# Performance work log

Hardware: AMD Instinct MI355X
Metric: run time of the kernel (lower is better)

## Reference

```python
import jax, jax.numpy as jnp
import numpy as np

BSZ, ILEN, TLEN = 64, 256, 64
IDIM, HDIM, ODIM = 512, 1024, 128


def setup_inputs() -> dict:
    key = jax.random.key(0)
    k1, k2, k3, k4 = jax.random.split(key, 4)
    # xavier-uniform-like scales (exact init values don't matter for correctness)
    def xavier(k, shape):
        fan_in, fan_out = shape[1], shape[0]
        lim = (6.0 / (fan_in + fan_out)) ** 0.5
        return jax.random.uniform(k, shape, jnp.float32, -lim, lim)
    return {
        "inp": jax.random.normal(k1, (BSZ, ILEN, IDIM), jnp.float32),
        "tlen": TLEN,
        "w_ih": xavier(k2, (4 * HDIM, IDIM)),
        "w_hh": xavier(k3, (4 * HDIM, HDIM)),
        "b": jnp.zeros((4 * HDIM,), jnp.float32),
        "clf_w": xavier(k4, (ODIM, HDIM)),
        "clf_b": jnp.zeros((ODIM,), jnp.float32),
    }


def _lstm_forward(inp, tlen, w_ih, w_hh, b, clf_w, clf_b):
    bsz, ilen, _ = inp.shape
    hdim = w_hh.shape[1]
    # pad tlen zero timesteps at the end (matches F.pad [0,0,0,tlen])
    inp_padded = jnp.pad(inp, ((0, 0), (0, tlen), (0, 0)))
    # precompute input projection for all timesteps: [B, T, 4H]
    x_proj = jnp.einsum("bti,gi->btg", inp_padded, w_ih) + b
    x_proj_t = jnp.swapaxes(x_proj, 0, 1)  # [T, B, 4H]

    def step(carry, xg):
        h, c = carry
        gates = xg + h @ w_hh.T  # [B, 4H]
        i, f, g, o = jnp.split(gates, 4, axis=-1)
        i = jax.nn.sigmoid(i)
        f = jax.nn.sigmoid(f)
        g = jnp.tanh(g)
        o = jax.nn.sigmoid(o)
        c_new = f * c + i * g
        h_new = o * jnp.tanh(c_new)
        return (h_new, c_new), h_new

    h0 = jnp.zeros((bsz, hdim), inp.dtype)
    c0 = jnp.zeros((bsz, hdim), inp.dtype)
    _, hs = jax.lax.scan(step, (h0, c0), x_proj_t)  # hs: [T, B, H]
    hs = jnp.swapaxes(hs, 0, 1)  # [B, T, H]
    probs = jax.nn.sigmoid(jnp.einsum("bth,oh->bto", hs, clf_w) + clf_b)
    return probs[:, ilen:]


def reference(inp, tlen, w_ih, w_hh, b, clf_w, clf_b):
    return _lstm_forward(inp, tlen, w_ih, w_hh, b, clf_w, clf_b)
```

## Files before the change

### kernel.cpp

```cpp
#include <hip/hip_runtime.h>
#include <hip/hip_bf16.h>

#define BSZ  64
#define ILEN 256
#define TLEN 64
#define TTOT (ILEN + TLEN)
#define IDIM 512
#define HDIM 1024
#define ODIM 128

#define NBLK 256
#define NTHR 512
#define NGRP 8
#define GBLK 32
#define UPB  32
#define NT   8
#define PN   132
#define HSLOT (BSZ * HDIM)

typedef __attribute__((ext_vector_type(8))) short short8;
typedef __attribute__((ext_vector_type(4))) float f32x4;
typedef _Float16 half_t;

__device__ inline ushort f2bf(float f) {
  unsigned u = __builtin_bit_cast(unsigned, f);
  u += 0x7fffu + ((u >> 16) & 1u);
  return (ushort)(u >> 16);
}

__device__ inline float fast_sigmoid(float x) {
  float e = __expf(-x);
  return 1.0f / (1.0f + e);
}
__device__ inline float fast_tanh(float x) {
  float e = __expf(2.0f * x);
  return 1.0f - 2.0f / (1.0f + e);
}

__device__ inline void st_h_sys(ushort* p, ushort v) {
  __hip_atomic_store(p, v, __ATOMIC_RELAXED, __HIP_MEMORY_SCOPE_SYSTEM);
}
__device__ inline void vm_drain() { asm volatile("s_waitcnt vmcnt(0)" ::: "memory"); }

template<bool FAST>
__device__ __forceinline__ int ldflag(const int* p) {
  if constexpr (FAST)
    return __hip_atomic_load(p, __ATOMIC_RELAXED, __HIP_MEMORY_SCOPE_AGENT);
  else
    return __hip_atomic_load(p, __ATOMIC_RELAXED, __HIP_MEMORY_SCOPE_SYSTEM);
}
template<bool FAST>
__device__ __forceinline__ void stflag(int* p, int v) {
  if constexpr (FAST)
    __hip_atomic_store(p, v, __ATOMIC_RELAXED, __HIP_MEMORY_SCOPE_AGENT);
  else
    __hip_atomic_store(p, v, __ATOMIC_RELAXED, __HIP_MEMORY_SCOPE_SYSTEM);
}

template<bool FAST>
__device__ __forceinline__ void ld_h4(const ushort* p, short8& a0, short8& a1,
                                      short8& a2, short8& a3) {
  if constexpr (FAST)
    asm volatile("global_load_dwordx4 %0, %4, off sc0\n\t"
                 "global_load_dwordx4 %1, %4, off offset:64 sc0\n\t"
                 "global_load_dwordx4 %2, %4, off offset:128 sc0\n\t"
                 "global_load_dwordx4 %3, %4, off offset:192 sc0\n\t"
                 "s_waitcnt vmcnt(0)"
                 : "=&v"(a0), "=&v"(a1), "=&v"(a2), "=&v"(a3)
                 : "v"(p) : "memory");
  else
    asm volatile("global_load_dwordx4 %0, %4, off sc0 sc1\n\t"
                 "global_load_dwordx4 %1, %4, off offset:64 sc0 sc1\n\t"
                 "global_load_dwordx4 %2, %4, off offset:128 sc0 sc1\n\t"
                 "global_load_dwordx4 %3, %4, off offset:192 sc0 sc1\n\t"
                 "s_waitcnt vmcnt(0)"
                 : "=&v"(a0), "=&v"(a1), "=&v"(a2), "=&v"(a3)
                 : "v"(p) : "memory");
}

__global__ void prep_kernel(const float* __restrict__ inp, const float* __restrict__ clfw,
                            const float* __restrict__ w_ih, const float* __restrict__ w_hh,
                            ushort* __restrict__ inp_bf, ushort* __restrict__ clfw_bf,
                            ushort* __restrict__ wih_bf, ushort* __restrict__ whh_sw,
                            ushort* __restrict__ hbuf, int* __restrict__ bar,
                            int* __restrict__ hand)
{
  const long np  = (long)gridDim.x * blockDim.x;
  const long tid = (long)blockIdx.x * blockDim.x + threadIdx.x;

  const float4* in4 = (const float4*)inp;
  ushort4* ob4 = (ushort4*)inp_bf;
  for (long i = tid; i < (long)BSZ * ILEN * IDIM / 4; i += np) {
    float4 v = in4[i];
    ushort4 o; o.x = f2bf(v.x); o.y = f2bf(v.y); o.z = f2bf(v.z); o.w = f2bf(v.w);
    ob4[i] = o;
  }
  const float4* cw4 = (const float4*)clfw;
  ushort4* cb4 = (ushort4*)clfw_bf;
  for (long i = tid; i < (long)ODIM * HDIM / 4; i += np) {
    float4 v = cw4[i];
    ushort4 o; o.x = f2bf(v.x); o.y = f2bf(v.y); o.z = f2bf(v.z); o.w = f2bf(v.w);
    cb4[i] = o;
  }
  const float4* wi4 = (const float4*)w_ih;
  ushort4* wb4 = (ushort4*)wih_bf;
  for (long i = tid; i < (long)4 * HDIM * IDIM / 4; i += np) {
    float4 v = wi4[i];
    ushort4 o; o.x = f2bf(v.x); o.y = f2bf(v.y); o.z = f2bf(v.z); o.w = f2bf(v.w);
    wb4[i] = o;
  }
  for (long f = tid; f < 32L * 8 * 4 * 8 * 64; f += np) {
    const int lane = (int)(f & 63);
    const int nt   = (int)((f >> 6) & 7);
    const int c    = (int)((f >> 9) & 3);
    const int wv   = (int)((f >> 11) & 7);
    const int r    = (int)(f >> 14);
    const int nl   = nt * 16 + (lane & 15);
    const long grow = (long)(nl >> 5) * HDIM + r * UPB + (nl & 31);
    const int k = wv * 128 + c * 32 + (lane >> 4) * 8;
    const float* src = w_hh + grow * HDIM + k;
    ushort* dst = whh_sw + f * 8;
    #pragma unroll
    for (int j = 0; j < 8; ++j) dst[j] = f2bf(src[j]);
  }
  for (long i = tid; i < (long)4 * HSLOT; i += np)
    st_h_sys(hbuf + i, 0);
  for (long i = tid; i < NBLK * 32; i += np)
    __hip_atomic_store(bar + (int)i, 0, __ATOMIC_RELAXED, __HIP_MEMORY_SCOPE_SYSTEM);
  for (long i = tid; i < 256; i += np)
    __hip_atomic_store(hand + (int)i, 0, __ATOMIC_RELAXED, __HIP_MEMORY_SCOPE_SYSTEM);
}

__global__ __launch_bounds__(256, 1) void xproj_kernel(
    const ushort* __restrict__ inp_bf, const ushort* __restrict__ wih_bf,
    half_t* __restrict__ xproj)
{
  const int tid = threadIdx.x;
  const int wv = tid >> 6, lane = tid & 63, l15 = lane & 15, quad = lane >> 4;
  const int mtile = blockIdx.x >> 6;
  const int ntile = blockIdx.x & 63;
  const int mb = mtile * 128 + wv * 32;
  const int nb = ntile * 64;

  f32x4 acc[2][4];
  #pragma unroll
  for (int mi = 0; mi < 2; ++mi)
    #pragma unroll
    for (int nt = 0; nt < 4; ++nt)
      #pragma unroll
      for (int r = 0; r < 4; ++r) acc[mi][nt][r] = 0.0f;

  for (int kc = 0; kc < IDIM / 32; ++kc) {
    const int k = kc * 32 + quad * 8;
    short8 a0 = *(const short8*)(inp_bf + (long)(mb + l15) * IDIM + k);
    short8 a1 = *(const short8*)(inp_bf + (long)(mb + 16 + l15) * IDIM + k);
    #pragma unroll
    for (int nt = 0; nt < 4; ++nt) {
      short8 b = *(const short8*)(wih_bf + (long)(nb + nt * 16 + l15) * IDIM + k);
      acc[0][nt] = __builtin_amdgcn_mfma_f32_16x16x32_bf16(a0, b, acc[0][nt], 0, 0, 0);
      acc[1][nt] = __builtin_amdgcn_mfma_f32_16x16x32_bf16(a1, b, acc[1][nt], 0, 0, 0);
    }
  }
  #pragma unroll
  for (int mi = 0; mi < 2; ++mi)
    #pragma unroll
    for (int nt = 0; nt < 4; ++nt)
      #pragma unroll
      for (int r = 0; r < 4; ++r) {
        const int m = mb + mi * 16 + quad * 4 + r;
        xproj[(long)m * (4 * HDIM) + nb + nt * 16 + l15] = (half_t)acc[mi][nt][r];
      }
}

template<bool FAST>
__device__ __forceinline__ void lstm_body(
    const ushort* __restrict__ whh_sw, const half_t* __restrict__ xproj,
    const float* __restrict__ bias, ushort* __restrict__ hbuf,
    ushort* __restrict__ hs_bf, int* __restrict__ flags)
{
  extern __shared__ float part[];

  const int tid  = threadIdx.x;
  const int wv   = tid >> 6;
  const int lane = tid & 63;
  const int l15  = lane & 15;
  const int quad = lane >> 4;
  const int blk  = blockIdx.x;
  const int g    = blk & 7;
  const int role = blk >> 3;
  const int j0u  = role * UPB;
  const int m0   = g * 8;

  short8 wfrag[4][NT];
  {
    const ushort* wp = whh_sw + (long)(role * 8 + wv) * 16384 + lane * 8;
    #pragma unroll
    for (int c = 0; c < 4; ++c)
      #pragma unroll
      for (int nt = 0; nt < NT; ++nt)
        wfrag[c][nt] = *(const short8*)(wp + (c * NT + nt) * 512);
  }
  #pragma unroll
  for (int c = 0; c < 4; ++c)
    #pragma unroll
    for (int nt = 0; nt < NT; ++nt)
      asm volatile("" : "+v"(wfrag[c][nt]));

  const int em = tid >> 5;
  const int uu = tid & 31;
  float bi = 0, bf_ = 0, bg = 0, bo = 0;
  const half_t* xgp = xproj + (long)(m0 + em) * ILEN * (4 * HDIM) + j0u + uu;
  if (tid < 256) {
    bi  = bias[0 * HDIM + j0u + uu];
    bf_ = bias[1 * HDIM + j0u + uu];
    bg  = bias[2 * HDIM + j0u + uu];
    bo  = bias[3 * HDIM + j0u + uu];
  }
  float cst = 0.0f;

  int* const fmine = flags + (g * GBLK + role) * 32;
  const int fidx = (lane < 4) ? (g * GBLK + wv * 4 + lane) : (g * GBLK + role);
  const int* const myfp = flags + fidx * 32;

  float xi = 0, xf = 0, xg = 0, xo = 0;
  if (tid < 256) {
    xi = (float)xgp[0 * HDIM]; xf = (float)xgp[1 * HDIM];
    xg = (float)xgp[2 * HDIM]; xo = (float)xgp[3 * HDIM];
  }

  for (int t = 0; t < TTOT; ++t) {
    const ushort* __restrict__ hsrc = hbuf + (t & 3) * HSLOT;
    ushort* __restrict__ hdst = hbuf + ((t + 1) & 3) * HSLOT;

    for (;;) {
      int v = ldflag<FAST>(myfp);
      if (__all(v >= t)) break;
      __builtin_amdgcn_s_sleep(1);
    }

    const ushort* hb = hsrc + (long)(m0 + (l15 & 7)) * HDIM + wv * 128 + quad * 8;
    short8 ah0, ah1, ah2, ah3;
    ld_h4<FAST>(hb, ah0, ah1, ah2, ah3);

    f32x4 acc[NT];
    #pragma unroll
    for (int nt = 0; nt < NT; ++nt)
      #pragma unroll
      for (int r = 0; r < 4; ++r) acc[nt][r] = 0.0f;

    #pragma unroll
    for (int nt = 0; nt < NT; ++nt)
      acc[nt] = __builtin_amdgcn_mfma_f32_16x16x32_bf16(ah0, wfrag[0][nt], acc[nt], 0, 0, 0);
    #pragma unroll
    for (int nt = 0; nt < NT; ++nt)
      acc[nt] = __builtin_amdgcn_mfma_f32_16x16x32_bf16(ah1, wfrag[1][nt], acc[nt], 0, 0, 0);
    #pragma unroll
    for (int nt = 0; nt < NT; ++nt)
      acc[nt] = __builtin_amdgcn_mfma_f32_16x16x32_bf16(ah2, wfrag[2][nt], acc[nt], 0, 0, 0);
    #pragma unroll
    for (int nt = 0; nt < NT; ++nt)
      acc[nt] = __builtin_amdgcn_mfma_f32_16x16x32_bf16(ah3, wfrag[3][nt], acc[nt], 0, 0, 0);

    if (quad < 2) {
      #pragma unroll
      for (int nt = 0; nt < NT; ++nt)
        #pragma unroll
        for (int r = 0; r < 4; ++r)
          part[(wv * 16 + quad * 4 + r) * PN + nt * 16 + l15] = acc[nt][r];
    }
    __syncthreads();

    ushort h16 = 0;
    if (tid < 256) {
      float gi = bi + xi, gf = bf_ + xf, gg = bg + xg, go = bo + xo;
      #pragma unroll
      for (int w = 0; w < 8; ++w) {
        const float* pw = part + (w * 16 + em) * PN;
        gi += pw[0 * 32 + uu];
        gf += pw[1 * 32 + uu];
        gg += pw[2 * 32 + uu];
        go += pw[3 * 32 + uu];
      }
      const float si = fast_sigmoid(gi);
      const float sf = fast_sigmoid(gf);
      const float tg = fast_tanh(gg);
      const float so = fast_sigmoid(go);
      cst = sf * cst + si * tg;
      const float h = so * fast_tanh(cst);
      h16 = f2bf(h);
      if constexpr (FAST)
        hdst[(long)(m0 + em) * HDIM + j0u + uu] = h16;
      else
        st_h_sys(hdst + (long)(m0 + em) * HDIM + j0u + uu, h16);
    }

    vm_drain();
    __syncthreads();
    if (tid == 0) stflag<FAST>(fmine, t + 1);

    if (tid < 256) {
      if (t >= ILEN)
        hs_bf[((long)(m0 + em) * TLEN + (t - ILEN)) * HDIM + j0u + uu] = h16;
      if (t + 1 < ILEN) {
        const half_t* xq = xgp + (long)(t + 1) * (4 * HDIM);
        xi = (float)xq[0 * HDIM]; xf = (float)xq[1 * HDIM];
        xg = (float)xq[2 * HDIM]; xo = (float)xq[3 * HDIM];
      } else {
        xi = xf = xg = xo = 0.0f;
      }
    }
  }
}

__global__ __launch_bounds__(NTHR, 2) void lstm_kernel(
    const ushort* __restrict__ whh_sw, const half_t* __restrict__ xproj,
    const float* __restrict__ bias,
    ushort* __restrict__ hbuf, ushort* __restrict__ hs_bf,
    int* __restrict__ flags, int* __restrict__ hand)
{
  int xcd = 0;
  asm volatile("s_getreg_b32 %0, hwreg(HW_REG_XCC_ID)" : "=s"(xcd));
  const int g = blockIdx.x & 7;
  if (threadIdx.x == 0) {
    __hip_atomic_fetch_or(&hand[g * 8], 1 << (xcd & 7),
                          __ATOMIC_RELAXED, __HIP_MEMORY_SCOPE_SYSTEM);
    __hip_atomic_fetch_add(&hand[64 + g * 8], 1,
                           __ATOMIC_RELAXED, __HIP_MEMORY_SCOPE_SYSTEM);
  }
  while (__hip_atomic_load(&hand[64 + g * 8], __ATOMIC_RELAXED,
                           __HIP_MEMORY_SCOPE_SYSTEM) < GBLK)
    __builtin_amdgcn_s_sleep(2);
  const bool fast =
      __popc(__hip_atomic_load(&hand[g * 8], __ATOMIC_RELAXED,
                               __HIP_MEMORY_SCOPE_SYSTEM)) == 1;

  if (fast) lstm_body<true >(whh_sw, xproj, bias, hbuf, hs_bf, flags);
  else      lstm_body<false>(whh_sw, xproj, bias, hbuf, hs_bf, flags);
}

__global__ __launch_bounds__(256, 1) void clf_kernel(
    const ushort* __restrict__ hs_bf, const ushort* __restrict__ clfw_bf,
    const float* __restrict__ clf_b, float* __restrict__ out)
{
  const int tid = threadIdx.x;
  const int wv = tid >> 6, lane = tid & 63, l15 = lane & 15, quad = lane >> 4;
  const int m0 = blockIdx.x * 64 + wv * 16;

  f32x4 acc[8];
  #pragma unroll
  for (int nt = 0; nt < 8; ++nt)
    #pragma unroll
    for (int r = 0; r < 4; ++r) acc[nt][r] = 0.0f;

  for (int kc = 0; kc < HDIM / 32; ++kc) {
    const int k = kc * 32 + quad * 8;
    short8 a = *(const short8*)(hs_bf + (long)(m0 + l15) * HDIM + k);
    #pragma unroll
    for (int nt = 0; nt < 8; ++nt) {
      short8 b = *(const short8*)(clfw_bf + (long)(nt * 16 + l15) * HDIM + k);
      acc[nt] = __builtin_amdgcn_mfma_f32_16x16x32_bf16(a, b, acc[nt], 0, 0, 0);
    }
  }
  #pragma unroll
  for (int nt = 0; nt < 8; ++nt) {
    const int n = nt * 16 + l15;
    const float bn = clf_b[n];
    #pragma unroll
    for (int r = 0; r < 4; ++r) {
      const int m = m0 + quad * 4 + r;
      out[(long)m * ODIM + n] = fast_sigmoid(acc[nt][r] + bn);
    }
  }
}

extern "C" void kernel_launch(void* const* d_in, const int* in_sizes, int n_in,
                              void* d_out, int out_size, void* d_ws, size_t ws_size,
                              hipStream_t stream) {
  const float* inp   = (const float*)d_in[0];
  const float* w_ih  = (const float*)d_in[2];
  const float* w_hh  = (const float*)d_in[3];
  const float* bias  = (const float*)d_in[4];
  const float* clf_w = (const float*)d_in[5];
  const float* clf_b = (const float*)d_in[6];
  float* out = (float*)d_out;

  char* ws = (char*)d_ws;
  ushort* inp_bf  = (ushort*)(ws + 0);
  ushort* wih_bf  = (ushort*)(ws + 16777216);
  ushort* whh_sw  = (ushort*)(ws + 20971520);
  ushort* clfw_bf = (ushort*)(ws + 29360128);
  ushort* hbuf    = (ushort*)(ws + 29622272);
  ushort* hs_bf   = (ushort*)(ws + 30146560);
  int*    bar     = (int*)   (ws + 38535168);
  int*    hand    = (int*)   (ws + 38567936);
  half_t* xproj   = (half_t*)(ws + 38568960);

  prep_kernel<<<4096, 256, 0, stream>>>(inp, clf_w, w_ih, w_hh,
                                        inp_bf, clfw_bf, wih_bf, whh_sw,
                                        hbuf, bar, hand);
  xproj_kernel<<<8192, 256, 0, stream>>>(inp_bf, wih_bf, xproj);
  lstm_kernel<<<NBLK, NTHR, 8 * 16 * PN * 4, stream>>>(whh_sw, xproj, bias,
                                                       hbuf, hs_bf, bar, hand);
  clf_kernel<<<64, 256, 0, stream>>>(hs_bf, clfw_bf, clf_b, out);
}
```

Measured before the change: 1.327 ms.

## Tile xproj GEMM through LDS and prefetch x-gates into LDS in LSTM loop

The input-projection GEMM now stages 128x32 tiles of A and B into shared memory with direct global-to-LDS loads. Each wave computes a 64x64 sub-tile, which raises operand reuse and halves the grid. Inside the recurrent kernel, the upper 256 threads prefetch the next step's x-projection into a double-buffered LDS area, so the gate threads no longer issue global loads on the critical path. The partial-sum layout is interleaved so each gate thread reads its four gate values with one vector load. The w_hh swizzle in prep also uses vectorized float4 loads. The cost is a larger LDS footprint, extra synchronisation in the xproj loop, and a hand-placed barrier and waitcnt.

```diff
diff --git a/kernel.cpp b/kernel.cpp
--- a/kernel.cpp
+++ b/kernel.cpp
@@ -17,6 +17,7 @@
 #define NT   8
 #define PN   132
 #define HSLOT (BSZ * HDIM)
+#define XBUFF (2 * 8 * 4 * 32)
 
 typedef __attribute__((ext_vector_type(8))) short short8;
 typedef __attribute__((ext_vector_type(4))) float f32x4;
@@ -78,6 +79,12 @@
                  : "v"(p) : "memory");
 }
 
+__device__ __forceinline__ void gload_lds16(const ushort* g, ushort* l) {
+  __builtin_amdgcn_global_load_lds(
+      (const __attribute__((address_space(1))) unsigned int*)g,
+      (__attribute__((address_space(3))) unsigned int*)l, 16, 0, 0);
+}
+
 __global__ void prep_kernel(const float* __restrict__ inp, const float* __restrict__ clfw,
                             const float* __restrict__ w_ih, const float* __restrict__ w_hh,
                             ushort* __restrict__ inp_bf, ushort* __restrict__ clfw_bf,
@@ -119,9 +126,14 @@
     const long grow = (long)(nl >> 5) * HDIM + r * UPB + (nl & 31);
     const int k = wv * 128 + c * 32 + (lane >> 4) * 8;
     const float* src = w_hh + grow * HDIM + k;
+    const float4 s0 = *(const float4*)(src);
+    const float4 s1 = *(const float4*)(src + 4);
+    ushort4 d0, d1;
+    d0.x = f2bf(s0.x); d0.y = f2bf(s0.y); d0.z = f2bf(s0.z); d0.w = f2bf(s0.w);
+    d1.x = f2bf(s1.x); d1.y = f2bf(s1.y); d1.z = f2bf(s1.z); d1.w = f2bf(s1.w);
     ushort* dst = whh_sw + f * 8;
-    #pragma unroll
-    for (int j = 0; j < 8; ++j) dst[j] = f2bf(src[j]);
+    *(ushort4*)(dst)     = d0;
+    *(ushort4*)(dst + 4) = d1;
   }
   for (long i = tid; i < (long)4 * HSLOT; i += np)
     st_h_sys(hbuf + i, 0);
@@ -131,44 +143,69 @@
     __hip_atomic_store(hand + (int)i, 0, __ATOMIC_RELAXED, __HIP_MEMORY_SCOPE_SYSTEM);
 }
 
-__global__ __launch_bounds__(256, 1) void xproj_kernel(
+__global__ __launch_bounds__(256, 2) void xproj_kernel(
     const ushort* __restrict__ inp_bf, const ushort* __restrict__ wih_bf,
     half_t* __restrict__ xproj)
 {
+  __shared__ ushort As[128 * 32];
+  __shared__ ushort Bs[128 * 32];
+
   const int tid = threadIdx.x;
   const int wv = tid >> 6, lane = tid & 63, l15 = lane & 15, quad = lane >> 4;
-  const int mtile = blockIdx.x >> 6;
-  const int ntile = blockIdx.x & 63;
-  const int mb = mtile * 128 + wv * 32;
-  const int nb = ntile * 64;
-
-  f32x4 acc[2][4];
+  const int bs = (blockIdx.x & 7) * 512 + (blockIdx.x >> 3);
+  const long mb = (long)(bs >> 5) * 128;
+  const long nb = (long)(bs & 31) * 128;
+  const int wr = wv >> 1, wc = wv & 1;
+
+  const int srow = wv * 32 + (lane >> 2);
+  const int scol = (lane & 3) * 8;
+  const ushort* ga = inp_bf + (mb + srow) * IDIM + scol;
+  const ushort* gb = wih_bf + (nb + srow) * IDIM + scol;
+  ushort* const la = As + wv * 32 * 32;
+  ushort* const lb = Bs + wv * 32 * 32;
+
+  f32x4 acc[4][4];
   #pragma unroll
-  for (int mi = 0; mi < 2; ++mi)
+  for (int mt = 0; mt < 4; ++mt)
     #pragma unroll
     for (int nt = 0; nt < 4; ++nt)
       #pragma unroll
-      for (int r = 0; r < 4; ++r) acc[mi][nt][r] = 0.0f;
+      for (int r = 0; r < 4; ++r) acc[mt][nt][r] = 0.0f;
 
   for (int kc = 0; kc < IDIM / 32; ++kc) {
-    const int k = kc * 32 + quad * 8;
-    short8 a0 = *(const short8*)(inp_bf + (long)(mb + l15) * IDIM + k);
-    short8 a1 = *(const short8*)(inp_bf + (long)(mb + 16 + l15) * IDIM + k);
-    #pragma unroll
-    for (int nt = 0; nt < 4; ++nt) {
-      short8 b = *(const short8*)(wih_bf + (long)(nb + nt * 16 + l15) * IDIM + k);
-      acc[0][nt] = __builtin_amdgcn_mfma_f32_16x16x32_bf16(a0, b, acc[0][nt], 0, 0, 0);
-      acc[1][nt] = __builtin_amdgcn_mfma_f32_16x16x32_bf16(a1, b, acc[1][nt], 0, 0, 0);
-    }
-  }
+    const int k = kc * 32;
+    gload_lds16(ga + k,             la);
+    gload_lds16(ga + 16 * IDIM + k, la + 16 * 32);
+    gload_lds16(gb + k,             lb);
+    gload_lds16(gb + 16 * IDIM + k, lb + 16 * 32);
+    asm volatile("s_waitcnt vmcnt(0)" ::: "memory");
+    __syncthreads();
+
+    short8 af[4], bf[4];
+    #pragma unroll
+    for (int mt = 0; mt < 4; ++mt)
+      af[mt] = *(const short8*)(As + (wr * 64 + mt * 16 + l15) * 32 + quad * 8);
+    #pragma unroll
+    for (int nt = 0; nt < 4; ++nt)
+      bf[nt] = *(const short8*)(Bs + (wc * 64 + nt * 16 + l15) * 32 + quad * 8);
+    #pragma unroll
+    for (int mt = 0; mt < 4; ++mt)
+      #pragma unroll
+      for (int nt = 0; nt < 4; ++nt)
+        acc[mt][nt] = __builtin_amdgcn_mfma_f32_16x16x32_bf16(af[mt], bf[nt],
+                                                              acc[mt][nt], 0, 0, 0);
+    __syncthreads();
+  }
+
   #pragma unroll
-  for (int mi = 0; mi < 2; ++mi)
+  for (int mt = 0; mt < 4; ++mt)
     #pragma unroll
     for (int nt = 0; nt < 4; ++nt)
       #pragma unroll
       for (int r = 0; r < 4; ++r) {
-        const int m = mb + mi * 16 + quad * 4 + r;
-        xproj[(long)m * (4 * HDIM) + nb + nt * 16 + l15] = (half_t)acc[mi][nt][r];
+        const long m = mb + wr * 64 + mt * 16 + quad * 4 + r;
+        const long n = nb + wc * 64 + nt * 16 + l15;
+        xproj[m * (4 * HDIM) + n] = (half_t)acc[mt][nt][r];
       }
 }
 
@@ -179,6 +216,7 @@
     ushort* __restrict__ hs_bf, int* __restrict__ flags)
 {
   extern __shared__ float part[];
+  float* const xbuf = part + 8 * 16 * PN;
 
   const int tid  = threadIdx.x;
   const int wv   = tid >> 6;
@@ -209,7 +247,6 @@
   const int em = tid >> 5;
   const int uu = tid & 31;
   float bi = 0, bf_ = 0, bg = 0, bo = 0;
-  const half_t* xgp = xproj + (long)(m0 + em) * ILEN * (4 * HDIM) + j0u + uu;
   if (tid < 256) {
     bi  = bias[0 * HDIM + j0u + uu];
     bf_ = bias[1 * HDIM + j0u + uu];
@@ -218,14 +255,25 @@
   }
   float cst = 0.0f;
 
+  const int lane4 = (tid - 256) & 255;
+  const int em4 = lane4 >> 5;
+  const int g4  = (lane4 >> 3) & 3;
+  const int u0  = (lane4 & 7) * 4;
+  const half_t* xsrc = xproj + (long)(m0 + em4) * ILEN * (4 * HDIM)
+                       + g4 * HDIM + j0u + u0;
+
   int* const fmine = flags + (g * GBLK + role) * 32;
   const int fidx = (lane < 4) ? (g * GBLK + wv * 4 + lane) : (g * GBLK + role);
   const int* const myfp = flags + fidx * 32;
 
-  float xi = 0, xf = 0, xg = 0, xo = 0;
-  if (tid < 256) {
-    xi = (float)xgp[0 * HDIM]; xf = (float)xgp[1 * HDIM];
-    xg = (float)xgp[2 * HDIM]; xo = (float)xgp[3 * HDIM];
+  if (tid >= 256) {
+    ushort4 x0 = *(const ushort4*)xsrc;
+    float4 v;
+    v.x = (float)__builtin_bit_cast(half_t, (ushort)x0.x);
+    v.y = (float)__builtin_bit_cast(half_t, (ushort)x0.y);
+    v.z = (float)__builtin_bit_cast(half_t, (ushort)x0.z);
+    v.w = (float)__builtin_bit_cast(half_t, (ushort)x0.w);
+    *(float4*)(xbuf + 0 * 1024 + em4 * 128 + g4 * 32 + u0) = v;
   }
 
   for (int t = 0; t < TTOT; ++t) {
@@ -242,6 +290,14 @@
     short8 ah0, ah1, ah2, ah3;
     ld_h4<FAST>(hb, ah0, ah1, ah2, ah3);
 
+    ushort4 xr;
+    const bool havex = (tid >= 256) && (t + 1 < ILEN);
+    if (havex) {
+      const ushort* xp = (const ushort*)(xsrc + (long)(t + 1) * (4 * HDIM));
+      asm volatile("global_load_dwordx2 %0, %1, off"
+                   : "=&v"(xr) : "v"(xp) : "memory");
+    }
+
     f32x4 acc[NT];
     #pragma unroll
     for (int nt = 0; nt < NT; ++nt)
@@ -263,23 +319,30 @@
 
     if (quad < 2) {
       #pragma unroll
-      for (int nt = 0; nt < NT; ++nt)
+      for (int nt = 0; nt < NT; ++nt) {
+        const int n = nt * 16 + l15;
+        const int col = (n & 31) * 4 + (n >> 5);
         #pragma unroll
         for (int r = 0; r < 4; ++r)
-          part[(wv * 16 + quad * 4 + r) * PN + nt * 16 + l15] = acc[nt][r];
-    }
-    __syncthreads();
+          part[(wv * 16 + quad * 4 + r) * PN + col] = acc[nt][r];
+      }
+    }
+
+    asm volatile("s_waitcnt lgkmcnt(0)" ::: "memory");
+    __builtin_amdgcn_s_barrier();
 
     ushort h16 = 0;
     if (tid < 256) {
+      float xi = 0, xf = 0, xg = 0, xo = 0;
+      if (t < ILEN) {
+        const float* xb = xbuf + (t & 1) * 1024 + em * 128 + uu;
+        xi = xb[0]; xf = xb[32]; xg = xb[64]; xo = xb[96];
+      }
       float gi = bi + xi, gf = bf_ + xf, gg = bg + xg, go = bo + xo;
       #pragma unroll
       for (int w = 0; w < 8; ++w) {
-        const float* pw = part + (w * 16 + em) * PN;
-        gi += pw[0 * 32 + uu];
-        gf += pw[1 * 32 + uu];
-        gg += pw[2 * 32 + uu];
-        go += pw[3 * 32 + uu];
+        const f32x4 pw = *(const f32x4*)(part + (w * 16 + em) * PN + uu * 4);
+        gi += pw[0]; gf += pw[1]; gg += pw[2]; go += pw[3];
       }
       const float si = fast_sigmoid(gi);
       const float sf = fast_sigmoid(gf);
@@ -292,23 +355,22 @@
         hdst[(long)(m0 + em) * HDIM + j0u + uu] = h16;
       else
         st_h_sys(hdst + (long)(m0 + em) * HDIM + j0u + uu, h16);
+    } else if (havex) {
+      asm volatile("s_waitcnt vmcnt(0)" ::: "memory");
+      float4 v;
+      v.x = (float)__builtin_bit_cast(half_t, (ushort)xr.x);
+      v.y = (float)__builtin_bit_cast(half_t, (ushort)xr.y);
+      v.z = (float)__builtin_bit_cast(half_t, (ushort)xr.z);
+      v.w = (float)__builtin_bit_cast(half_t, (ushort)xr.w);
+      *(float4*)(xbuf + ((t + 1) & 1) * 1024 + em4 * 128 + g4 * 32 + u0) = v;
     }
 
     vm_drain();
     __syncthreads();
     if (tid == 0) stflag<FAST>(fmine, t + 1);
 
-    if (tid < 256) {
-      if (t >= ILEN)
-        hs_bf[((long)(m0 + em) * TLEN + (t - ILEN)) * HDIM + j0u + uu] = h16;
-      if (t + 1 < ILEN) {
-        const half_t* xq = xgp + (long)(t + 1) * (4 * HDIM);
-        xi = (float)xq[0 * HDIM]; xf = (float)xq[1 * HDIM];
-        xg = (float)xq[2 * HDIM]; xo = (float)xq[3 * HDIM];
-      } else {
-        xi = xf = xg = xo = 0.0f;
-      }
-    }
+    if (tid < 256 && t >= ILEN)
+      hs_bf[((long)(m0 + em) * TLEN + (t - ILEN)) * HDIM + j0u + uu] = h16;
   }
 }
 
@@ -398,8 +460,8 @@
   prep_kernel<<<4096, 256, 0, stream>>>(inp, clf_w, w_ih, w_hh,
                                         inp_bf, clfw_bf, wih_bf, whh_sw,
                                         hbuf, bar, hand);
-  xproj_kernel<<<8192, 256, 0, stream>>>(inp_bf, wih_bf, xproj);
-  lstm_kernel<<<NBLK, NTHR, 8 * 16 * PN * 4, stream>>>(whh_sw, xproj, bias,
-                                                       hbuf, hs_bf, bar, hand);
+  xproj_kernel<<<4096, 256, 0, stream>>>(inp_bf, wih_bf, xproj);
+  lstm_kernel<<<NBLK, NTHR, (8 * 16 * PN + XBUFF) * 4, stream>>>(
+      whh_sw, xproj, bias, hbuf, hs_bf, bar, hand);
   clf_kernel<<<64, 256, 0, stream>>>(hs_bf, clfw_bf, clf_b, out);
 }
```

Measured after the change: 1.144 ms. -13.8%, faster.
